# Performance work log

Hardware: AMD Instinct MI355X
Metric: run time of the kernel (lower is better)

## Reference

```python
import jax, jax.numpy as jnp
import numpy as np

B, C_IN, C_OUT, H, W = 16, 256, 256, 96, 96
HEADS, HEAD_DIM = 8, 32
PH, PW = 2, 2
M = PH * PW  # num prototypes


def _l2norm(v, axis=-1):
    return v / jnp.maximum(jnp.linalg.norm(v, axis=axis, keepdims=True), 1e-12)


def setup_inputs() -> dict:
    key = jax.random.key(0)
    ks = jax.random.split(key, 8)
    D = HEADS * HEAD_DIM
    x = jax.random.normal(ks[0], (B, C_IN, H, W), dtype=jnp.float32)
    s = 1.0 / np.sqrt(C_IN)
    Wf = jax.random.uniform(ks[1], (D, C_IN), minval=-s, maxval=s, dtype=jnp.float32)
    bf = jax.random.uniform(ks[2], (D,), minval=-s, maxval=s, dtype=jnp.float32)
    Wv = jax.random.uniform(ks[3], (D, C_IN), minval=-s, maxval=s, dtype=jnp.float32)
    bv = jax.random.uniform(ks[4], (D,), minval=-s, maxval=s, dtype=jnp.float32)
    sp = 1.0 / np.sqrt(D)
    Wp = jax.random.uniform(ks[5], (C_OUT, D), minval=-sp, maxval=sp, dtype=jnp.float32)
    bp = jax.random.uniform(ks[6], (C_OUT,), minval=-sp, maxval=sp, dtype=jnp.float32)
    # OrthogonalPriorGenerator: Gram-Schmidt orthonormal rows (frozen, requires_grad=False)
    rng = np.random.default_rng(0)
    W0 = rng.standard_normal((HEAD_DIM, M)).astype(np.float32)
    q, _ = np.linalg.qr(W0)  # [HEAD_DIM, M] orthonormal columns
    centers = jnp.asarray(q.T, dtype=jnp.float32)  # [M, HEAD_DIM], orthonormal rows
    sim_alpha = jnp.ones((1,), dtype=jnp.float32)
    sim_beta = jnp.zeros((1,), dtype=jnp.float32)
    return {"x": x, "Wf": Wf, "bf": bf, "Wv": Wv, "bv": bv, "Wp": Wp, "bp": bp,
            "sim_alpha": sim_alpha, "sim_beta": sim_beta, "centers": centers}


def reference(x, Wf, bf, Wv, bv, Wp, bp, sim_alpha, sim_beta, centers):
    Bx = x.shape[0]
    BE = Bx * HEADS
    N = H * W
    # 1x1 convs f and v
    value = jnp.einsum('bchw,oc->bohw', x, Wv) + bv[None, :, None, None]
    feat = jnp.einsum('bchw,oc->bohw', x, Wf) + bf[None, :, None, None]
    # split heads: b (e c) h w -> (b e) c h w
    value = value.reshape(BE, HEAD_DIM, H, W)
    feat = feat.reshape(BE, HEAD_DIM, H, W)
    # adaptive avg pool value to (PH, PW) -> [be, M, d]
    vc = value.reshape(BE, HEAD_DIM, PH, H // PH, PW, W // PW).mean(axis=(3, 5))
    value_centers = vc.reshape(BE, HEAD_DIM, M).transpose(0, 2, 1)  # [be, M, d]
    pix = feat.reshape(BE, HEAD_DIM, N).transpose(0, 2, 1)  # [be, N, d]
    # cosine similarity + sigmoid gate
    cn = _l2norm(centers)               # [M, d]
    pn = _l2norm(pix)                   # [be, N, d]
    sim = jax.nn.sigmoid(sim_beta + sim_alpha * jnp.einsum('md,bnd->bmn', cn, pn))  # [be, M, N]
    # top-1 hard assignment mask
    idx = jnp.argmax(sim, axis=1)                                   # [be, N]
    mask = jax.nn.one_hot(idx, M, axis=1, dtype=sim.dtype)          # [be, M, N]
    sim = sim * mask
    # weighted aggregate to cluster centers
    v2 = value.reshape(BE, HEAD_DIM, N).transpose(0, 2, 1)          # [be, N, d]
    agg = (jnp.einsum('bmn,bnd->bmd', sim, v2) + value_centers) / (sim.sum(axis=-1, keepdims=True) + 1.0)
    # dispatch back to pixels
    out = jnp.einsum('bmn,bmd->bnd', sim, agg)                      # [be, N, d]
    out = out.transpose(0, 2, 1).reshape(Bx, HEADS * HEAD_DIM, H, W)
    out = jnp.einsum('bchw,oc->bohw', out, Wp) + bp[None, :, None, None]
    assignment_map = idx[0].reshape(H, W)  # detached int map in original
    return out, assignment_map
```

## Files before the change

kernel.cpp:

```cpp
#include <hip/hip_runtime.h>
#include <hip/hip_bf16.h>

#define BB 16
#define CIN 256
#define DD 256
#define HH 96
#define NPIX 9216
#define HEADS 8
#define HD 32
#define MM 4
#define NT 144

typedef short bf16x8 __attribute__((ext_vector_type(8)));
typedef float f32x4 __attribute__((ext_vector_type(4)));

__device__ __forceinline__ float b2f(unsigned u) {
    unsigned x = u << 16;
    return __builtin_bit_cast(float, x);
}
__device__ __forceinline__ ushort f2b(float f) {
    unsigned x = __builtin_bit_cast(unsigned, f);
    unsigned r = (x + 0x7FFF + ((x >> 16) & 1)) >> 16;
    return (ushort)r;
}
__device__ __forceinline__ void gload16(const ushort* g, ushort* l) {
    __builtin_amdgcn_global_load_lds(
        (const __attribute__((address_space(1))) unsigned int*)g,
        (__attribute__((address_space(3))) unsigned int*)l, 16, 0, 0);
}

__global__ __launch_bounds__(256) void wprep_kernel(const float* __restrict__ Wf,
                                                    const float* __restrict__ Wv,
                                                    const float* __restrict__ bfp,
                                                    const float* __restrict__ centers,
                                                    ushort* __restrict__ wb,
                                                    float* __restrict__ GT,
                                                    float* __restrict__ gb) {
    __shared__ float cns[4][32];
    int t = threadIdx.x;
    if (blockIdx.x < 128) {
        int i = (blockIdx.x * 256 + t) * 4;
        float4 v;
        if (i < 65536) v = *(const float4*)(Wf + i);
        else v = *(const float4*)(Wv + (i - 65536));
        ushort4 o;
        o.x = f2b(v.x); o.y = f2b(v.y); o.z = f2b(v.z); o.w = f2b(v.w);
        *(ushort4*)(wb + i) = o;
        return;
    }
    if (t < 4) {
        float c[32]; float s = 0.f;
        for (int d = 0; d < 32; ++d) { c[d] = centers[t * 32 + d]; s += c[d] * c[d]; }
        float inv = 1.f / fmaxf(sqrtf(s), 1e-12f);
        for (int d = 0; d < 32; ++d) cns[t][d] = c[d] * inv;
    }
    __syncthreads();
    int i = (blockIdx.x - 128) * 256 + t;
    int c = i >> 5, em = i & 31;
    int e = em >> 2, m = em & 3;
    float s = 0.f;
#pragma unroll 8
    for (int d = 0; d < 32; ++d) s += cns[m][d] * Wf[(e * 32 + d) * 256 + c];
    GT[i] = s;
    if (blockIdx.x == 128 && t < 32) {
        int e2 = t >> 2, m2 = t & 3;
        float sb = 0.f;
        for (int d = 0; d < 32; ++d) sb += cns[m2][d] * bfp[e2 * 32 + d];
        gb[t] = sb;
    }
}

__global__ __launch_bounds__(256) void gmap_kernel(const float* __restrict__ x,
                                                   const float* __restrict__ GT,
                                                   const float* __restrict__ gb,
                                                   const float* __restrict__ alpha_p,
                                                   unsigned char* __restrict__ idxg,
                                                   float* __restrict__ zbest,
                                                   float* __restrict__ mapo) {
    int b = blockIdx.y;
    int emh = blockIdx.z;
    int t = threadIdx.x;
    int n = blockIdx.x * 256 + t;
    float acc[16];
#pragma unroll
    for (int em = 0; em < 16; ++em) acc[em] = gb[emh * 16 + em];
    const float* xb = x + (size_t)b * CIN * NPIX + n;
    const float* gtb = GT + emh * 16;
#pragma unroll 8
    for (int c = 0; c < 256; ++c) {
        float xv = xb[(size_t)c * NPIX];
        const float* gr = gtb + c * 32;
#pragma unroll
        for (int em = 0; em < 16; ++em) acc[em] = fmaf(gr[em], xv, acc[em]);
    }
    float alpha = alpha_p[0];
#pragma unroll
    for (int h = 0; h < 4; ++h) {
        int e = emh * 4 + h;
        float z0 = alpha * acc[h * 4 + 0], z1 = alpha * acc[h * 4 + 1];
        float z2 = alpha * acc[h * 4 + 2], z3 = alpha * acc[h * 4 + 3];
        int bm = 0; float bz = z0;
        if (z1 > bz) { bz = z1; bm = 1; }
        if (z2 > bz) { bz = z2; bm = 2; }
        if (z3 > bz) { bz = z3; bm = 3; }
        size_t o = ((size_t)(b * 8 + e)) * NPIX + n;
        idxg[o] = (unsigned char)bm;
        zbest[o] = bz;
        if (b == 0 && emh == 0 && h == 0) mapo[n] = (float)bm;
    }
}

__global__ __launch_bounds__(256, 2) void gemm_fvc(const ushort* __restrict__ wb,
                                                   const float* __restrict__ bfp,
                                                   const float* __restrict__ bvp,
                                                   const float* __restrict__ x,
                                                   const unsigned char* __restrict__ idxg,
                                                   float* __restrict__ zsg,
                                                   const float* __restrict__ beta_p,
                                                   float* __restrict__ partial2) {
    __shared__ ushort lB[64 * 256];
    __shared__ ushort lA[256 * 32];
    int nt = blockIdx.x, b = blockIdx.y;
    int t = threadIdx.x;
    int wave = t >> 6, lane = t & 63;
    int l15 = lane & 15, g8 = (lane >> 4) * 8, rg = lane >> 4;
    int n0 = nt * 64;

    {
        int cpl = 2 * (t & 31);
        int j0 = (t >> 5) * 8;
#pragma unroll
        for (int s = 0; s < 4; ++s) {
            int c0 = s * 64 + cpl;
            const float* xr = x + ((size_t)(b * CIN + c0)) * NPIX + n0 + j0;
            float4 u0 = *(const float4*)(xr);
            float4 u1 = *(const float4*)(xr + 4);
            float4 v0 = *(const float4*)(xr + NPIX);
            float4 v1 = *(const float4*)(xr + NPIX + 4);
            float a0[8] = {u0.x, u0.y, u0.z, u0.w, u1.x, u1.y, u1.z, u1.w};
            float a1[8] = {v0.x, v0.y, v0.z, v0.w, v1.x, v1.y, v1.z, v1.w};
#pragma unroll
            for (int i = 0; i < 8; ++i) {
                int n = j0 + i;
                int cs = c0 ^ ((n & 7) << 3);
                unsigned pk = (unsigned)f2b(a0[i]) | ((unsigned)f2b(a1[i]) << 16);
                *(unsigned*)(lB + (size_t)n * 256 + cs) = pk;
            }
        }
    }
    __syncthreads();

    float beta = beta_p[0];
    int mq[4];
#pragma unroll
    for (int j = 0; j < 4; ++j) {
        int n = n0 + j * 16 + l15;
        int hh = n / HH, ww = n - hh * HH;
        mq[j] = ((hh >= 48) ? 2 : 0) + ((ww >= 48) ? 1 : 0);
    }

    const ushort* aBase = wb + (t >> 2) * 256 + (t & 3) * 8;
    ushort* la0 = lA + wave * 512;

    f32x4 acc[4][4] = {};
    for (int kk = 0; kk < 8; ++kk) {
        int k0 = kk * 32;
        const ushort* aSrc = aBase;
        gload16(aSrc + k0, la0);
        gload16(aSrc + 64 * 256 + k0, la0 + 2048);
        gload16(aSrc + 128 * 256 + k0, la0 + 4096);
        gload16(aSrc + 192 * 256 + k0, la0 + 6144);
        __syncthreads();
        bf16x8 af[4], bb[4];
#pragma unroll
        for (int i = 0; i < 4; ++i)
            af[i] = *(const bf16x8*)(lA + (wave * 64 + i * 16 + l15) * 32 + g8);
#pragma unroll
        for (int j = 0; j < 4; ++j) {
            int n = j * 16 + l15;
            int cs = (k0 + g8) ^ ((n & 7) << 3);
            bb[j] = *(const bf16x8*)(lB + (size_t)n * 256 + cs);
        }
#pragma unroll
        for (int i = 0; i < 4; ++i)
#pragma unroll
            for (int j = 0; j < 4; ++j)
                acc[i][j] = __builtin_amdgcn_mfma_f32_16x16x32_bf16(af[i], bb[j], acc[i][j], 0, 0, 0);
        __syncthreads();
    }
#pragma unroll
    for (int i = 0; i < 4; ++i) {
        int cc = wave * 64 + i * 16 + rg * 4;
        float q0 = bfp[cc], q1 = bfp[cc + 1], q2 = bfp[cc + 2], q3 = bfp[cc + 3];
#pragma unroll
        for (int j = 0; j < 4; ++j) {
            acc[i][j][0] += q0; acc[i][j][1] += q1; acc[i][j][2] += q2; acc[i][j][3] += q3;
        }
    }
    float sg[2][4]; int bmv[2][4]; float wm[2][4][4];
#pragma unroll
    for (int h = 0; h < 2; ++h) {
        int e = wave * 2 + h;
#pragma unroll
        for (int j = 0; j < 4; ++j) {
            float nr = 0.f;
#pragma unroll
            for (int i2 = 0; i2 < 2; ++i2) {
                int i = h * 2 + i2;
#pragma unroll
                for (int r = 0; r < 4; ++r) nr += acc[i][j][r] * acc[i][j][r];
            }
            nr += __shfl_xor(nr, 16);
            nr += __shfl_xor(nr, 32);
            size_t o = ((size_t)(b * 8 + e)) * NPIX + n0 + j * 16 + l15;
            float z = zsg[o];
            int bm = idxg[o];
            float inv = 1.f / fmaxf(sqrtf(nr), 1e-12f);
            float s = 1.f / (1.f + __expf(-(beta + z * inv)));
            sg[h][j] = s; bmv[h][j] = bm;
            if (rg == 0) zsg[o] = s;
#pragma unroll
            for (int m = 0; m < 4; ++m)
                wm[h][j][m] = ((bm == m) ? s : 0.f) + ((mq[j] == m) ? (1.f / 2304.f) : 0.f);
        }
    }

    f32x4 acc2[4][4] = {};
    for (int kk = 0; kk < 8; ++kk) {
        int k0 = kk * 32;
        const ushort* aSrc = aBase + 65536;
        gload16(aSrc + k0, la0);
        gload16(aSrc + 64 * 256 + k0, la0 + 2048);
        gload16(aSrc + 128 * 256 + k0, la0 + 4096);
        gload16(aSrc + 192 * 256 + k0, la0 + 6144);
        __syncthreads();
        bf16x8 af[4], bb[4];
#pragma unroll
        for (int i = 0; i < 4; ++i)
            af[i] = *(const bf16x8*)(lA + (wave * 64 + i * 16 + l15) * 32 + g8);
#pragma unroll
        for (int j = 0; j < 4; ++j) {
            int n = j * 16 + l15;
            int cs = (k0 + g8) ^ ((n & 7) << 3);
            bb[j] = *(const bf16x8*)(lB + (size_t)n * 256 + cs);
        }
#pragma unroll
        for (int i = 0; i < 4; ++i)
#pragma unroll
            for (int j = 0; j < 4; ++j)
                acc2[i][j] = __builtin_amdgcn_mfma_f32_16x16x32_bf16(af[i], bb[j], acc2[i][j], 0, 0, 0);
        __syncthreads();
    }
#pragma unroll
    for (int i = 0; i < 4; ++i) {
        int cc = wave * 64 + i * 16 + rg * 4;
        float q0 = bvp[cc], q1 = bvp[cc + 1], q2 = bvp[cc + 2], q3 = bvp[cc + 3];
#pragma unroll
        for (int j = 0; j < 4; ++j) {
            acc2[i][j][0] += q0; acc2[i][j][1] += q1; acc2[i][j][2] += q2; acc2[i][j][3] += q3;
        }
    }
#pragma unroll
    for (int h = 0; h < 2; ++h) {
        int e = wave * 2 + h;
        float* prow = partial2 + ((size_t)(b * 8 + e) * NT + nt) * 132;
#pragma unroll
        for (int m = 0; m < 4; ++m) {
            float s = 0.f;
#pragma unroll
            for (int j = 0; j < 4; ++j) s += (bmv[h][j] == m) ? sg[h][j] : 0.f;
            s += __shfl_xor(s, 1); s += __shfl_xor(s, 2);
            s += __shfl_xor(s, 4); s += __shfl_xor(s, 8);
            if (lane == 0) prow[128 + m] = s;
        }
#pragma unroll
        for (int i2 = 0; i2 < 2; ++i2) {
            int i = h * 2 + i2;
#pragma unroll
            for (int m = 0; m < 4; ++m) {
                float sv[4];
#pragma unroll
                for (int r = 0; r < 4; ++r) {
                    float s = wm[h][0][m] * acc2[i][0][r] + wm[h][1][m] * acc2[i][1][r]
                            + wm[h][2][m] * acc2[i][2][r] + wm[h][3][m] * acc2[i][3][r];
                    s += __shfl_xor(s, 1); s += __shfl_xor(s, 2);
                    s += __shfl_xor(s, 4); s += __shfl_xor(s, 8);
                    sv[r] = s;
                }
                if (l15 == 0) {
                    int d0 = i2 * 16 + rg * 4;
                    *(float4*)(prow + m * 32 + d0) = make_float4(sv[0], sv[1], sv[2], sv[3]);
                }
            }
        }
    }
}

__global__ __launch_bounds__(256) void psum_kernel(const float* __restrict__ partial2,
                                                   float* __restrict__ tot) {
    int be = blockIdx.x;
    int t = threadIdx.x;
    if (t >= 132) return;
    const float* p = partial2 + (size_t)be * NT * 132 + t;
    float s = 0.f;
#pragma unroll 16
    for (int k = 0; k < NT; ++k) s += p[(size_t)k * 132];
    tot[be * 132 + t] = s;
}

__global__ __launch_bounds__(256) void agg_pa_kernel(const float* __restrict__ tot,
                                                     const float* __restrict__ Wp,
                                                     ushort* __restrict__ PAb) {
    __shared__ float aggs[8][4][32];
    __shared__ float tmp[136];
    int b = blockIdx.x;
    int t = threadIdx.x;
    for (int e = 0; e < 8; ++e) {
        int be = b * 8 + e;
        if (t < 132) tmp[t] = tot[be * 132 + t];
        __syncthreads();
        if (t < 128) aggs[e][t >> 5][t & 31] = tmp[t] / (tmp[128 + (t >> 5)] + 1.0f);
        __syncthreads();
    }
    const float* wrow = Wp + (size_t)t * 256;
    unsigned u[16];
#pragma unroll
    for (int k = 0; k < 16; ++k) {
        float s0 = 0.f, s1 = 0.f;
        int em0 = 2 * k, em1 = 2 * k + 1;
        int e0 = em0 >> 2, m0 = em0 & 3;
        int e1 = em1 >> 2, m1 = em1 & 3;
#pragma unroll
        for (int d = 0; d < 32; ++d) {
            s0 += wrow[e0 * 32 + d] * aggs[e0][m0][d];
            s1 += wrow[e1 * 32 + d] * aggs[e1][m1][d];
        }
        u[k] = (unsigned)f2b(s0) | ((unsigned)f2b(s1) << 16);
    }
    uint4* pab = (uint4*)(PAb + (size_t)b * 8192 + (size_t)t * 32);
    pab[0] = make_uint4(u[0], u[1], u[2], u[3]);
    pab[1] = make_uint4(u[4], u[5], u[6], u[7]);
    pab[2] = make_uint4(u[8], u[9], u[10], u[11]);
    pab[3] = make_uint4(u[12], u[13], u[14], u[15]);
}

__global__ __launch_bounds__(256) void gemm_out(const ushort* __restrict__ PAb,
                                                const float* __restrict__ sgv,
                                                const unsigned char* __restrict__ idxg,
                                                const float* __restrict__ bpp,
                                                float* __restrict__ out) {
    int nt = blockIdx.x, b = blockIdx.y;
    int t = threadIdx.x, wave = t >> 6, lane = t & 63;
    int wr = wave >> 1, wc = wave & 1;
    int l15 = lane & 15, kg = lane >> 4;
    const ushort* pab = PAb + (size_t)b * 8192;
    bf16x8 af[8];
#pragma unroll
    for (int i = 0; i < 8; ++i)
        af[i] = *(const bf16x8*)(pab + (size_t)(wr * 128 + i * 16 + l15) * 32 + kg * 8);
    int e0 = kg * 2;
    bf16x8 bb[4];
#pragma unroll
    for (int j = 0; j < 4; ++j) {
        int gn = nt * 128 + wc * 64 + j * 16 + l15;
        size_t ofs0 = ((size_t)(b * 8 + e0)) * NPIX + gn;
        float s0 = sgv[ofs0];
        float s1 = sgv[ofs0 + NPIX];
        int i0 = idxg[ofs0];
        int i1 = idxg[ofs0 + NPIX];
        unsigned h0 = f2b(s0), h1 = f2b(s1);
        unsigned w0 = (i0 & 1) ? (h0 << 16) : h0;
        unsigned w1 = (i1 & 1) ? (h1 << 16) : h1;
        uint4 q;
        q.x = (i0 >> 1) ? 0u : w0;
        q.y = (i0 >> 1) ? w0 : 0u;
        q.z = (i1 >> 1) ? 0u : w1;
        q.w = (i1 >> 1) ? w1 : 0u;
        bb[j] = __builtin_bit_cast(bf16x8, q);
    }
    f32x4 acc[8][4] = {};
#pragma unroll
    for (int i = 0; i < 8; ++i)
#pragma unroll
        for (int j = 0; j < 4; ++j)
            acc[i][j] = __builtin_amdgcn_mfma_f32_16x16x32_bf16(af[i], bb[j], acc[i][j], 0, 0, 0);
#pragma unroll
    for (int i = 0; i < 8; ++i) {
        int o0 = wr * 128 + i * 16 + kg * 4;
        float4 bi = *(const float4*)(bpp + o0);
#pragma unroll
        for (int j = 0; j < 4; ++j) {
            int gn = nt * 128 + wc * 64 + j * 16 + l15;
            size_t base = ((size_t)(b * 256 + o0)) * NPIX + gn;
            out[base] = acc[i][j][0] + bi.x;
            out[base + (size_t)NPIX] = acc[i][j][1] + bi.y;
            out[base + 2 * (size_t)NPIX] = acc[i][j][2] + bi.z;
            out[base + 3 * (size_t)NPIX] = acc[i][j][3] + bi.w;
        }
    }
}

extern "C" void kernel_launch(void* const* d_in, const int* in_sizes, int n_in,
                              void* d_out, int out_size, void* d_ws, size_t ws_size,
                              hipStream_t stream) {
    const float* x   = (const float*)d_in[0];
    const float* Wf  = (const float*)d_in[1];
    const float* bfp = (const float*)d_in[2];
    const float* Wv  = (const float*)d_in[3];
    const float* bvp = (const float*)d_in[4];
    const float* Wp  = (const float*)d_in[5];
    const float* bpp = (const float*)d_in[6];
    const float* al  = (const float*)d_in[7];
    const float* bt  = (const float*)d_in[8];
    const float* ce  = (const float*)d_in[9];
    float* out = (float*)d_out;

    char* ws = (char*)d_ws;
    float*  partial2 = (float*)ws;
    ushort* wbuf = (ushort*)(ws + 75497472);
    float*  GT   = (float*)(ws + 75759616);
    float*  gb   = (float*)(ws + 75792384);
    unsigned char* idxg = (unsigned char*)(ws + 75792640);
    float*  zbest = (float*)(ws + 76972288);
    float*  tot   = (float*)(ws + 81690880);
    ushort* PAb   = (ushort*)(ws + 82317568);

    float* mapo = out + (size_t)BB * DD * NPIX;

    wprep_kernel<<<dim3(160), 256, 0, stream>>>(Wf, Wv, bfp, ce, wbuf, GT, gb);
    gmap_kernel<<<dim3(36, BB, 2), 256, 0, stream>>>(x, GT, gb, al, idxg, zbest, mapo);
    gemm_fvc<<<dim3(NT, BB), 256, 0, stream>>>(wbuf, bfp, bvp, x, idxg, zbest, bt, partial2);
    psum_kernel<<<dim3(128), 256, 0, stream>>>(partial2, tot);
    agg_pa_kernel<<<dim3(BB), 256, 0, stream>>>(tot, Wp, PAb);
    gemm_out<<<dim3(72, BB), 256, 0, stream>>>(PAb, zbest, idxg, bpp, out);
}
```

Before: 205.8 us.

## Double-buffer per-wave weight tiles and drop block barriers in gemm_fvc K-loops

Each wave now loads only its own 64 rows of weight tiles into a private LDS region with two buffers. The next K-step is prefetched asynchronously and waited on with s_waitcnt vmcnt instead of __syncthreads, and the prefetch runs across from the f GEMM into the v GEMM. This removes the block-wide barriers and hides global load latency behind MFMA work. In exchange LDS use doubles for lA, and correctness now depends on the vmcnt counting and on gload16 writes being visible within the wave without a barrier.

```diff
diff --git a/kernel.cpp b/kernel.cpp
--- a/kernel.cpp
+++ b/kernel.cpp
@@ -119,7 +119,7 @@
                                                    const float* __restrict__ beta_p,
                                                    float* __restrict__ partial2) {
     __shared__ ushort lB[64 * 256];
-    __shared__ ushort lA[256 * 32];
+    __shared__ ushort lA[2 * 4 * 2048];
     int nt = blockIdx.x, b = blockIdx.y;
     int t = threadIdx.x;
     int wave = t >> 6, lane = t & 63;
@@ -148,7 +148,6 @@
             }
         }
     }
-    __syncthreads();
 
     float beta = beta_p[0];
     int mq[4];
@@ -159,22 +158,34 @@
         mq[j] = ((hh >= 48) ? 2 : 0) + ((ww >= 48) ? 1 : 0);
     }
 
-    const ushort* aBase = wb + (t >> 2) * 256 + (t & 3) * 8;
-    ushort* la0 = lA + wave * 512;
+    const ushort* aLane = wb + (size_t)(wave * 64 + (lane >> 2)) * 256 + (lane & 3) * 8;
+    ushort* laW0 = lA + wave * 2048;
+    ushort* laW1 = lA + 8192 + wave * 2048;
+
+#pragma unroll
+    for (int i = 0; i < 4; ++i)
+        gload16(aLane + (size_t)(i * 16) * 256, laW0 + i * 512);
+
+    __syncthreads();
 
     f32x4 acc[4][4] = {};
     for (int kk = 0; kk < 8; ++kk) {
+        {
+            size_t gofs = (kk == 7) ? 65536 : 0;
+            int k0n = (kk == 7) ? 0 : (kk + 1) * 32;
+            ushort* dst = ((kk + 1) & 1) ? laW1 : laW0;
+#pragma unroll
+            for (int i = 0; i < 4; ++i)
+                gload16(aLane + gofs + (size_t)(i * 16) * 256 + k0n, dst + i * 512);
+        }
+        asm volatile("s_waitcnt vmcnt(4)" ::: "memory");
+        __builtin_amdgcn_sched_barrier(0);
         int k0 = kk * 32;
-        const ushort* aSrc = aBase;
-        gload16(aSrc + k0, la0);
-        gload16(aSrc + 64 * 256 + k0, la0 + 2048);
-        gload16(aSrc + 128 * 256 + k0, la0 + 4096);
-        gload16(aSrc + 192 * 256 + k0, la0 + 6144);
-        __syncthreads();
+        const ushort* laB = (kk & 1) ? laW1 : laW0;
         bf16x8 af[4], bb[4];
 #pragma unroll
         for (int i = 0; i < 4; ++i)
-            af[i] = *(const bf16x8*)(lA + (wave * 64 + i * 16 + l15) * 32 + g8);
+            af[i] = *(const bf16x8*)(laB + (i * 16 + l15) * 32 + g8);
 #pragma unroll
         for (int j = 0; j < 4; ++j) {
             int n = j * 16 + l15;
@@ -186,7 +197,6 @@
 #pragma unroll
             for (int j = 0; j < 4; ++j)
                 acc[i][j] = __builtin_amdgcn_mfma_f32_16x16x32_bf16(af[i], bb[j], acc[i][j], 0, 0, 0);
-        __syncthreads();
     }
 #pragma unroll
     for (int i = 0; i < 4; ++i) {
@@ -227,17 +237,23 @@
 
     f32x4 acc2[4][4] = {};
     for (int kk = 0; kk < 8; ++kk) {
+        if (kk < 7) {
+            int k0n = (kk + 1) * 32;
+            ushort* dst = ((kk + 1) & 1) ? laW1 : laW0;
+#pragma unroll
+            for (int i = 0; i < 4; ++i)
+                gload16(aLane + 65536 + (size_t)(i * 16) * 256 + k0n, dst + i * 512);
+            asm volatile("s_waitcnt vmcnt(4)" ::: "memory");
+        } else {
+            asm volatile("s_waitcnt vmcnt(0)" ::: "memory");
+        }
+        __builtin_amdgcn_sched_barrier(0);
         int k0 = kk * 32;
-        const ushort* aSrc = aBase + 65536;
-        gload16(aSrc + k0, la0);
-        gload16(aSrc + 64 * 256 + k0, la0 + 2048);
-        gload16(aSrc + 128 * 256 + k0, la0 + 4096);
-        gload16(aSrc + 192 * 256 + k0, la0 + 6144);
-        __syncthreads();
+        const ushort* laB = (kk & 1) ? laW1 : laW0;
         bf16x8 af[4], bb[4];
 #pragma unroll
         for (int i = 0; i < 4; ++i)
-            af[i] = *(const bf16x8*)(lA + (wave * 64 + i * 16 + l15) * 32 + g8);
+            af[i] = *(const bf16x8*)(laB + (i * 16 + l15) * 32 + g8);
 #pragma unroll
         for (int j = 0; j < 4; ++j) {
             int n = j * 16 + l15;
@@ -249,7 +265,6 @@
 #pragma unroll
             for (int j = 0; j < 4; ++j)
                 acc2[i][j] = __builtin_amdgcn_mfma_f32_16x16x32_bf16(af[i], bb[j], acc2[i][j], 0, 0, 0);
-        __syncthreads();
     }
 #pragma unroll
     for (int i = 0; i < 4; ++i) {
```

After: 191.0 us. 7.2% less time.

## Pre-swizzle weights into MFMA fragment order and load A directly from global

Applied to the files above, without the earlier changes.

The weight-prep kernel now writes the bf16 weights in a per-wave, per-k-chunk MFMA fragment layout. The GEMM loops can then load A fragments straight from global memory (L2-resident) instead of staging them through LDS with global_load_lds, which removes the lA buffer and both __syncthreads per k-iteration. The smaller LDS footprint allows launch bounds of 4 blocks per CU, and x packing uses the hardware v_cvt_pk_bf16_f32 instruction. The trade-off is more global/L2 load traffic per wave and higher register pressure from the fully unrolled loops under the tighter occupancy bound.

```diff
diff --git a/kernel.cpp b/kernel.cpp
--- a/kernel.cpp
+++ b/kernel.cpp
@@ -23,10 +23,10 @@
     unsigned r = (x + 0x7FFF + ((x >> 16) & 1)) >> 16;
     return (ushort)r;
 }
-__device__ __forceinline__ void gload16(const ushort* g, ushort* l) {
-    __builtin_amdgcn_global_load_lds(
-        (const __attribute__((address_space(1))) unsigned int*)g,
-        (__attribute__((address_space(3))) unsigned int*)l, 16, 0, 0);
+__device__ __forceinline__ unsigned cvtpk(float lo, float hi) {
+    unsigned r;
+    asm("v_cvt_pk_bf16_f32 %0, %1, %2" : "=v"(r) : "v"(lo), "v"(hi));
+    return r;
 }
 
 __global__ __launch_bounds__(256) void wprep_kernel(const float* __restrict__ Wf,
@@ -39,13 +39,19 @@
     __shared__ float cns[4][32];
     int t = threadIdx.x;
     if (blockIdx.x < 128) {
-        int i = (blockIdx.x * 256 + t) * 4;
+        int idx = (blockIdx.x * 256 + t) * 4;
         float4 v;
-        if (i < 65536) v = *(const float4*)(Wf + i);
-        else v = *(const float4*)(Wv + (i - 65536));
+        if (idx < 65536) v = *(const float4*)(Wf + idx);
+        else v = *(const float4*)(Wv + (idx - 65536));
+        int g = idx >> 16;
+        int rem = idx & 65535;
+        int rr = rem >> 8, k0 = rem & 255;
+        int w = rr >> 6, i = (rr >> 4) & 3, l15v = rr & 15;
+        int kk = k0 >> 5, lane4 = ((k0 >> 3) & 3) * 16 + l15v, j = k0 & 7;
+        size_t dst = ((size_t)((g * 8 + kk) * 4 + w)) * 2048 + (i * 64 + lane4) * 8 + j;
         ushort4 o;
         o.x = f2b(v.x); o.y = f2b(v.y); o.z = f2b(v.z); o.w = f2b(v.w);
-        *(ushort4*)(wb + i) = o;
+        *(ushort4*)(wb + dst) = o;
         return;
     }
     if (t < 4) {
@@ -110,7 +116,7 @@
     }
 }
 
-__global__ __launch_bounds__(256, 2) void gemm_fvc(const ushort* __restrict__ wb,
+__global__ __launch_bounds__(256, 4) void gemm_fvc(const ushort* __restrict__ wb,
                                                    const float* __restrict__ bfp,
                                                    const float* __restrict__ bvp,
                                                    const float* __restrict__ x,
@@ -119,7 +125,6 @@
                                                    const float* __restrict__ beta_p,
                                                    float* __restrict__ partial2) {
     __shared__ ushort lB[64 * 256];
-    __shared__ ushort lA[256 * 32];
     int nt = blockIdx.x, b = blockIdx.y;
     int t = threadIdx.x;
     int wave = t >> 6, lane = t & 63;
@@ -143,12 +148,11 @@
             for (int i = 0; i < 8; ++i) {
                 int n = j0 + i;
                 int cs = c0 ^ ((n & 7) << 3);
-                unsigned pk = (unsigned)f2b(a0[i]) | ((unsigned)f2b(a1[i]) << 16);
+                unsigned pk = cvtpk(a0[i], a1[i]);
                 *(unsigned*)(lB + (size_t)n * 256 + cs) = pk;
             }
         }
     }
-    __syncthreads();
 
     float beta = beta_p[0];
     int mq[4];
@@ -159,22 +163,17 @@
         mq[j] = ((hh >= 48) ? 2 : 0) + ((ww >= 48) ? 1 : 0);
     }
 
-    const ushort* aBase = wb + (t >> 2) * 256 + (t & 3) * 8;
-    ushort* la0 = lA + wave * 512;
+    __syncthreads();
 
     f32x4 acc[4][4] = {};
+#pragma unroll
     for (int kk = 0; kk < 8; ++kk) {
+        const ushort* aCh = wb + (size_t)(kk * 4 + wave) * 2048;
         int k0 = kk * 32;
-        const ushort* aSrc = aBase;
-        gload16(aSrc + k0, la0);
-        gload16(aSrc + 64 * 256 + k0, la0 + 2048);
-        gload16(aSrc + 128 * 256 + k0, la0 + 4096);
-        gload16(aSrc + 192 * 256 + k0, la0 + 6144);
-        __syncthreads();
         bf16x8 af[4], bb[4];
 #pragma unroll
         for (int i = 0; i < 4; ++i)
-            af[i] = *(const bf16x8*)(lA + (wave * 64 + i * 16 + l15) * 32 + g8);
+            af[i] = *(const bf16x8*)(aCh + (i * 64 + lane) * 8);
 #pragma unroll
         for (int j = 0; j < 4; ++j) {
             int n = j * 16 + l15;
@@ -186,7 +185,6 @@
 #pragma unroll
             for (int j = 0; j < 4; ++j)
                 acc[i][j] = __builtin_amdgcn_mfma_f32_16x16x32_bf16(af[i], bb[j], acc[i][j], 0, 0, 0);
-        __syncthreads();
     }
 #pragma unroll
     for (int i = 0; i < 4; ++i) {
@@ -226,18 +224,14 @@
     }
 
     f32x4 acc2[4][4] = {};
+#pragma unroll
     for (int kk = 0; kk < 8; ++kk) {
+        const ushort* aCh = wb + (size_t)((8 + kk) * 4 + wave) * 2048;
         int k0 = kk * 32;
-        const ushort* aSrc = aBase + 65536;
-        gload16(aSrc + k0, la0);
-        gload16(aSrc + 64 * 256 + k0, la0 + 2048);
-        gload16(aSrc + 128 * 256 + k0, la0 + 4096);
-        gload16(aSrc + 192 * 256 + k0, la0 + 6144);
-        __syncthreads();
         bf16x8 af[4], bb[4];
 #pragma unroll
         for (int i = 0; i < 4; ++i)
-            af[i] = *(const bf16x8*)(lA + (wave * 64 + i * 16 + l15) * 32 + g8);
+            af[i] = *(const bf16x8*)(aCh + (i * 64 + lane) * 8);
 #pragma unroll
         for (int j = 0; j < 4; ++j) {
             int n = j * 16 + l15;
@@ -249,7 +243,6 @@
 #pragma unroll
             for (int j = 0; j < 4; ++j)
                 acc2[i][j] = __builtin_amdgcn_mfma_f32_16x16x32_bf16(af[i], bb[j], acc2[i][j], 0, 0, 0);
-        __syncthreads();
     }
 #pragma unroll
     for (int i = 0; i < 4; ++i) {
```

After: 225.7 us. 9.7% more time.
